# Kernel optimization log

Measured on AMD Instinct MI355X. Metric: run time of the kernel, lower is better.

Reference implementation:

```python
import jax, jax.numpy as jnp
import numpy as np

SEQ, B, IN, H = 256, 64, 1024, 1024
P_IN, P_HID = 0.3, 0.3


def setup_inputs() -> dict:
    key = jax.random.key(0)
    ks = jax.random.split(key, 8)
    bound = 1.0 / np.sqrt(H)
    # variational dropout masks: Bernoulli(keep)/keep, sampled once, reused every step
    keep_x, keep_h = 1.0 - P_IN, 1.0 - P_HID
    mask_x = (jax.random.uniform(ks[0], (B, IN)) < keep_x).astype(jnp.float32) / keep_x
    mask_h = (jax.random.uniform(ks[1], (B, H)) < keep_h).astype(jnp.float32) / keep_h
    return {
        "x": jax.random.normal(ks[2], (SEQ, B, IN), jnp.float32),
        "h0": jax.random.normal(ks[3], (B, H), jnp.float32),
        "c0": jax.random.normal(ks[4], (B, H), jnp.float32),
        "mask_x": mask_x,
        "mask_h": mask_h,
        "W_ih": jax.random.uniform(ks[5], (4 * H, IN), jnp.float32, -bound, bound),
        "W_hh": jax.random.uniform(ks[6], (4 * H, H), jnp.float32, -bound, bound),
        "b_ih": jax.random.uniform(ks[7], (4 * H,), jnp.float32, -bound, bound),
        "b_hh": jax.random.uniform(jax.random.fold_in(key, 9), (4 * H,), jnp.float32, -bound, bound),
    }


def reference(x, h0, c0, mask_x, mask_h, W_ih, W_hh, b_ih, b_hh):
    # input dropout mask applied once to all timesteps, then input gate
    # projections precomputed in one big GEMM: [S, B, 4H]
    x_gates = jnp.einsum('sbi,gi->sbg', x * mask_x[None], W_ih) + (b_ih + b_hh)

    def step(carry, xg):
        h, c = carry
        # hidden dropout mask applied to h before the cell, every step
        gates = xg + (h * mask_h) @ W_hh.T  # [B, 4H]
        i, f, g, o = jnp.split(gates, 4, axis=-1)  # torch LSTM gate order
        i = jax.nn.sigmoid(i)
        f = jax.nn.sigmoid(f)
        g = jnp.tanh(g)
        o = jax.nn.sigmoid(o)
        c_new = f * c + i * g
        h_new = o * jnp.tanh(c_new)
        return (h_new, c_new), h_new

    (h_n, c_n), output = jax.lax.scan(step, (h0, c0), x_gates)
    return output, h_n, c_n
```

## Files before the change

kernel.cpp:

```cpp
#include <hip/hip_runtime.h>
#include <stdint.h>
#include <stddef.h>


#define SEQ 256

typedef __attribute__((ext_vector_type(8))) __bf16 bf16x8;
typedef __attribute__((ext_vector_type(4))) float  f32x4;
typedef __attribute__((ext_vector_type(4))) _Float16 f16x4;
typedef __attribute__((ext_vector_type(4))) unsigned int u32x4;
typedef unsigned short u16;
typedef unsigned int   u32;
typedef unsigned long long u64;

__device__ __forceinline__ u16 f2bf(float f) {
  union { float f; unsigned u; } v; v.f = f;
  unsigned r = v.u + 0x7FFFu + ((v.u >> 16) & 1u);
  return (u16)(r >> 16);
}
__device__ __forceinline__ float sigm(float x) {
  return __builtin_amdgcn_rcpf(1.f + __expf(-x));
}
__device__ __forceinline__ float tanh_fast(float x) {
  float xc = fminf(15.f, fmaxf(-15.f, x));
  float t = __expf(-2.f * xc);
  return (1.f - t) * __builtin_amdgcn_rcpf(1.f + t);
}
__device__ __forceinline__ float pick4(int idx, float v0, float v1, float v2, float v3) {
  float lo = (idx & 1) ? v1 : v0;
  float hi = (idx & 1) ? v3 : v2;
  return (idx & 2) ? hi : lo;
}


__global__ __launch_bounds__(256) void prep_kernel(
    const float* __restrict__ x, const float* __restrict__ h0,
    const float* __restrict__ c0, const float* __restrict__ mask_x,
    const float* __restrict__ mask_h, const float* __restrict__ Wih,
    const float* __restrict__ Whh, const float* __restrict__ bih,
    const float* __restrict__ bhh,
    u16* __restrict__ Wihp, u16* __restrict__ Whhp, u16* __restrict__ Ap,
    u16* __restrict__ mhp0, float* __restrict__ bias, float* __restrict__ c,
    u32* __restrict__ flags, int persist)
{
  const unsigned t    = blockIdx.x * 256u + threadIdx.x;
  const unsigned idx8 = t * 8u;

  union Pack8 { u16 o[8]; u32x4 v; };

  {
    const unsigned l   = (idx8 >> 3) & 63u;
    const unsigned kwg = (idx8 >> 9) & 31u;
    const unsigned m   = (idx8 >> 14) & 3u;
    const unsigned s   = idx8 >> 16;
    const unsigned b   = m * 16u + (l & 15u);
    const unsigned k   = kwg * 32u + (l >> 4) * 8u;
    const float* xp = &x[((size_t)s * 64u + b) * 1024u + k];
    const float* mp = &mask_x[b * 1024u + k];
    Pack8 p;
    #pragma unroll
    for (int e = 0; e < 8; ++e) p.o[e] = f2bf(xp[e] * mp[e]);
    *(u32x4*)&Ap[idx8] = p.v;
  }
  if (t < 524288u) {
    const unsigned l   = (idx8 >> 3) & 63u;
    const unsigned kcw = (idx8 >> 9) & 31u;
    const unsigned wb  = idx8 >> 14;
    const unsigned nl  = l & 15u;
    const unsigned n   = (nl & 3u) * 1024u + wb * 4u + (nl >> 2);
    const unsigned k   = kcw * 32u + (l >> 4) * 8u;
    const float* wip = &Wih[n * 1024u + k];
    const float* whp = &Whh[n * 1024u + k];
    Pack8 pi, ph;
    #pragma unroll
    for (int e = 0; e < 8; ++e) { pi.o[e] = f2bf(wip[e]); ph.o[e] = f2bf(whp[e]); }
    *(u32x4*)&Wihp[idx8] = pi.v;
    *(u32x4*)&Whhp[idx8] = ph.v;
  }
  if (t < 8192u) {
    const unsigned l   = (idx8 >> 3) & 63u;
    const unsigned kwg = (idx8 >> 9) & 31u;
    const unsigned m   = idx8 >> 14;
    const unsigned b   = m * 16u + (l & 15u);
    const unsigned k   = kwg * 32u + (l >> 4) * 8u;
    const float* hp = &h0[b * 1024u + k];
    const float* mp = &mask_h[b * 1024u + k];
    Pack8 p;
    #pragma unroll
    for (int e = 0; e < 8; ++e) p.o[e] = f2bf(hp[e] * mp[e]);
    *(u32x4*)&mhp0[idx8] = p.v;
    *(f32x4*)&c[idx8]     = *(const f32x4*)&c0[idx8];
    *(f32x4*)&c[idx8 + 4] = *(const f32x4*)&c0[idx8 + 4];
  }
  if (t < 512u) {
    #pragma unroll
    for (int e = 0; e < 8; ++e) bias[idx8 + e] = bih[idx8 + e] + bhh[idx8 + e];
  }
  if (persist && t < 256u) flags[t] = 0u;
}

__global__ __launch_bounds__(512) void lstm_persist(
    const u16* __restrict__ Ap, const u16* __restrict__ Wihp,
    const u16* __restrict__ Whhp, const float* __restrict__ bias,
    const float* __restrict__ c0, const float* __restrict__ mask_h,
    u16* __restrict__ mh_seq,
    u32* __restrict__ flags, float* __restrict__ out)
{
  __shared__ f32x4 lds[8][4][64];
  __shared__ u32 cnt;

  const int tid = threadIdx.x;
  const int w   = tid >> 6;
  const int l   = tid & 63;
  const int bk  = blockIdx.x;
  const int rg  = bk >> 6;
  const int cg  = bk & 63;

  const bf16x8* WHV = (const bf16x8*)Whhp;
  const bf16x8* WIV = (const bf16x8*)Wihp;
  const bf16x8* ApV = (const bf16x8*)Ap;

  bf16x8 wh[4][4], wi[4][4];
  #pragma unroll
  for (int nt = 0; nt < 4; ++nt)
    #pragma unroll
    for (int kw = 0; kw < 4; ++kw) {
      wh[nt][kw] = WHV[((cg * 4 + nt) * 32 + w * 4 + kw) * 64 + l];
      wi[nt][kw] = WIV[((cg * 4 + nt) * 32 + w * 4 + kw) * 64 + l];
    }

  const int nl     = l & 15;
  const int quad   = l >> 4;
  const int g_role = nl & 3;
  const int jh     = nl >> 2;

  const int nt_e  = w & 3;
  const int rb    = (w >> 2) * 2;
  const int col_h = cg * 16 + nt_e * 4 + jh;
  const float bias_reg = bias[g_role * 1024 + col_h];
  float c_reg[2], mask_reg[2];
  #pragma unroll
  for (int rl = 0; rl < 2; ++rl) {
    const int row = rg * 16 + quad * 4 + rb + rl;
    c_reg[rl]    = c0[row * 1024 + col_h];
    mask_reg[rl] = mask_h[row * 1024 + col_h];
  }

  const int mh_u16_base =
      ((rg * 32 + (cg >> 1)) * 64 + ((cg & 1) * 2 + (nt_e >> 1)) * 16 + quad * 4) * 8
      + (nt_e & 1) * 4;

  const u32 poll_off = (u32)((rg * 64 + w * 8 + (l & 7)) * 4);

  if (tid == 0) cnt = 0u;
  __syncthreads();

  for (int s = 0; s < SEQ; ++s) {
    const u16* mi = mh_seq + (size_t)s * 65536;
    u16*       mo = mh_seq + (size_t)(s + 1) * 65536;

    f32x4 acc[4];
    #pragma unroll
    for (int nt = 0; nt < 4; ++nt) acc[nt] = (f32x4){0.f, 0.f, 0.f, 0.f};
    #pragma unroll
    for (int kw = 0; kw < 4; ++kw) {
      bf16x8 a = ApV[((s * 4 + rg) * 32 + w * 4 + kw) * 64 + l];
      #pragma unroll
      for (int nt = 0; nt < 4; ++nt)
        acc[nt] = __builtin_amdgcn_mfma_f32_16x16x32_bf16(a, wi[nt][kw], acc[nt], 0, 0, 0);
    }

    if (s > 0) {
      const u32 target = (u32)s;
      int spins = 0;
      for (;;) {
        u32 f;
        asm volatile("global_load_dword %0, %1, %2 sc0 sc1\n\t"
                     "s_waitcnt vmcnt(0)"
                     : "=v"(f) : "v"(poll_off), "s"(flags) : "memory");
        if (__all(f >= target)) break;
        if (++spins > (1 << 15)) break;
        __builtin_amdgcn_s_sleep(1);
      }
    }

    union { u32x4 r; bf16x8 v; } hf[4];
    #pragma unroll
    for (int kw = 0; kw < 4; ++kw) {
      const u32 off = (u32)(((rg * 32 + w * 4 + kw) * 64 + l) * 16);
      asm volatile("global_load_dwordx4 %0, %1, %2 sc0 sc1"
                   : "=v"(hf[kw].r) : "v"(off), "s"(mi) : "memory");
    }
    asm volatile("s_waitcnt vmcnt(0)" ::: "memory");
    __builtin_amdgcn_sched_barrier(0);
    #pragma unroll
    for (int kw = 0; kw < 4; ++kw)
      #pragma unroll
      for (int nt = 0; nt < 4; ++nt)
        acc[nt] = __builtin_amdgcn_mfma_f32_16x16x32_bf16(hf[kw].v, wh[nt][kw], acc[nt], 0, 0, 0);

    #pragma unroll
    for (int nt = 0; nt < 4; ++nt) lds[w][nt][l] = acc[nt];
    __syncthreads();

    f32x4 t = lds[0][nt_e][l];
    #pragma unroll
    for (int ww = 1; ww < 8; ++ww) t += lds[ww][nt_e][l];

    f32x4 ho_s[2];
    f32x4 co_s[2];
    #pragma unroll
    for (int rl = 0; rl < 2; ++rl) {
      const int r = rb + rl;
      const float gp = t[r] + bias_reg;
      const float v1 = __shfl_xor(gp, 1, 64);
      const float v2 = __shfl_xor(gp, 2, 64);
      const float v3 = __shfl_xor(gp, 3, 64);
      const float ig = pick4(g_role,     gp, v1, v2, v3);
      const float fg = pick4(g_role ^ 1, gp, v1, v2, v3);
      const float gg = pick4(g_role ^ 2, gp, v1, v2, v3);
      const float og = pick4(g_role ^ 3, gp, v1, v2, v3);
      const float iv = sigm(ig);
      const float fv = sigm(fg);
      const float gv = tanh_fast(gg);
      const float ov = sigm(og);
      const float cn = fv * c_reg[rl] + iv * gv;
      c_reg[rl] = cn;
      const float hn = ov * tanh_fast(cn);
      const float mv = hn * mask_reg[rl];

      const float h1 = __shfl_xor(hn, 4, 64);
      const float h2 = __shfl_xor(hn, 8, 64);
      const float h3 = __shfl_xor(hn, 12, 64);
      const float m1 = __shfl_xor(mv, 4, 64);
      const float m2 = __shfl_xor(mv, 8, 64);
      const float m3 = __shfl_xor(mv, 12, 64);
      ho_s[rl] = (f32x4){hn, h1, h2, h3};
      if (s == SEQ - 1) {
        const float cn1 = __shfl_xor(cn, 4, 64);
        const float cn2 = __shfl_xor(cn, 8, 64);
        const float cn3 = __shfl_xor(cn, 12, 64);
        co_s[rl] = (f32x4){cn, cn1, cn2, cn3};
      }
      if (nl == 0) {
        const u64 pk = (u64)f2bf(mv) | ((u64)f2bf(m1) << 16)
                     | ((u64)f2bf(m2) << 32) | ((u64)f2bf(m3) << 48);
        __hip_atomic_store((u64*)&mo[mh_u16_base + r * 8], pk,
                           __ATOMIC_RELAXED, __HIP_MEMORY_SCOPE_AGENT);
      }
    }
    asm volatile("s_waitcnt vmcnt(0)" ::: "memory");
    u32 old = 0u;
    if (l == 0)
      old = __hip_atomic_fetch_add(&cnt, 1u, __ATOMIC_RELAXED, __HIP_MEMORY_SCOPE_WORKGROUP);
    if (l == 0 && old == 7u) {
      __hip_atomic_store(&cnt, 0u, __ATOMIC_RELAXED, __HIP_MEMORY_SCOPE_WORKGROUP);
      if (s < SEQ - 1) {
        u32 val  = (u32)(s + 1);
        u32 voff = (u32)(bk * 4);
        asm volatile("global_store_dword %0, %1, %2 sc0 sc1"
                     :: "v"(voff), "v"(val), "s"(flags) : "memory");
      }
    }
    if (nl == 0) {
      #pragma unroll
      for (int rl = 0; rl < 2; ++rl) {
        const int row = rg * 16 + quad * 4 + rb + rl;
        *(f32x4*)&out[((size_t)s * 64 + row) * 1024 + cg * 16 + nt_e * 4] = ho_s[rl];
        if (s == SEQ - 1) {
          *(f32x4*)&out[16777216 + row * 1024 + cg * 16 + nt_e * 4] = ho_s[rl];
          *(f32x4*)&out[16777216 + 65536 + row * 1024 + cg * 16 + nt_e * 4] = co_s[rl];
        }
      }
    }
    __syncthreads();
  }
}

__global__ __launch_bounds__(256) void lstm_step(
    const u16* __restrict__ Ap,
    const u16* __restrict__ Wihp,
    const u16* __restrict__ Whhp,
    const _Float16* __restrict__ xg,
    const float* __restrict__ bias,
    const u16* __restrict__ mh_in, u16* __restrict__ mh_out,
    float* __restrict__ c, const float* __restrict__ mask_h,
    float* __restrict__ out, int s)
{
  __shared__ f32x4 lds[4][4][64];

  const int tid = threadIdx.x;
  const int w   = tid >> 6;
  const int l   = tid & 63;
  const int bk  = blockIdx.x;

  const bf16x8* mb = (const bf16x8*)mh_in;
  const bf16x8* WH = (const bf16x8*)Whhp;

  f32x4 acc[4] = { {0,0,0,0}, {0,0,0,0}, {0,0,0,0}, {0,0,0,0} };

  #pragma unroll 2
  for (int kw = 0; kw < 8; ++kw) {
    bf16x8 b = WH[(bk * 32 + w * 8 + kw) * 64 + l];
    #pragma unroll
    for (int m = 0; m < 4; ++m) {
      bf16x8 a = mb[(m * 32 + w * 8 + kw) * 64 + l];
      acc[m] = __builtin_amdgcn_mfma_f32_16x16x32_bf16(a, b, acc[m], 0, 0, 0);
    }
  }
  if (xg == nullptr) {
    const bf16x8* ApV = (const bf16x8*)Ap;
    const bf16x8* WI  = (const bf16x8*)Wihp;
    #pragma unroll 2
    for (int kw = 0; kw < 8; ++kw) {
      bf16x8 b = WI[(bk * 32 + w * 8 + kw) * 64 + l];
      #pragma unroll
      for (int m = 0; m < 4; ++m) {
        bf16x8 a = ApV[((s * 4 + m) * 32 + w * 8 + kw) * 64 + l];
        acc[m] = __builtin_amdgcn_mfma_f32_16x16x32_bf16(a, b, acc[m], 0, 0, 0);
      }
    }
  }
  #pragma unroll
  for (int m = 0; m < 4; ++m) lds[w][m][l] = acc[m];
  __syncthreads();

  f32x4 t = lds[0][w][l];
  #pragma unroll
  for (int ww = 1; ww < 4; ++ww) t += lds[ww][w][l];

  const int nl     = l & 15;
  const int quad   = l >> 4;
  const int g_role = nl & 3;
  const int jh     = nl >> 2;
  const int col_h  = bk * 4 + jh;

  if (xg != nullptr) {
    f16x4 xv = *(const f16x4*)&xg[((((size_t)s * 256 + bk) * 4 + w) * 64 + l) * 4];
    #pragma unroll
    for (int r = 0; r < 4; ++r) t[r] += (float)xv[r];
  }
  const float bias_reg = bias[g_role * 1024 + col_h];
  const int kwg = col_h >> 5;
  const int lp  = ((col_h >> 3) & 3) * 16;

  #pragma unroll
  for (int r = 0; r < 4; ++r) {
    const int b_row = w * 16 + quad * 4 + r;
    const float gp = t[r] + bias_reg;
    const float v1 = __shfl_xor(gp, 1, 64);
    const float v2 = __shfl_xor(gp, 2, 64);
    const float v3 = __shfl_xor(gp, 3, 64);
    const float ig = pick4(g_role,     gp, v1, v2, v3);
    const float fg = pick4(g_role ^ 1, gp, v1, v2, v3);
    const float gg = pick4(g_role ^ 2, gp, v1, v2, v3);
    const float og = pick4(g_role ^ 3, gp, v1, v2, v3);
    const float iv = sigm(ig);
    const float fv = sigm(fg);
    const float gv = tanh_fast(gg);
    const float ov = sigm(og);
    const float cold = c[b_row * 1024 + col_h];
    const float cn = fv * cold + iv * gv;
    const float hn = ov * tanh_fast(cn);
    if (g_role == 0) {
      c[b_row * 1024 + col_h] = cn;
      out[((size_t)s * 64 + b_row) * 1024 + col_h] = hn;
      mh_out[((w * 32 + kwg) * 64 + (lp + (b_row & 15))) * 8 + (col_h & 7)] =
          f2bf(hn * mask_h[b_row * 1024 + col_h]);
      if (s == SEQ - 1) {
        out[16777216 + b_row * 1024 + col_h] = hn;
        out[16777216 + 65536 + b_row * 1024 + col_h] = cn;
      }
    }
  }
}

extern "C" void kernel_launch(void* const* d_in, const int* in_sizes, int n_in,
                              void* d_out, int out_size, void* d_ws, size_t ws_size,
                              hipStream_t stream)
{
  const float* x      = (const float*)d_in[0];
  const float* h0     = (const float*)d_in[1];
  const float* c0     = (const float*)d_in[2];
  const float* mask_x = (const float*)d_in[3];
  const float* mask_h = (const float*)d_in[4];
  const float* Wih    = (const float*)d_in[5];
  const float* Whh    = (const float*)d_in[6];
  const float* bih    = (const float*)d_in[7];
  const float* bhh    = (const float*)d_in[8];
  float* out = (float*)d_out;

  char* ws = (char*)d_ws;
  u16*   Wihp   = (u16*)(ws + 0);
  u16*   Whhp   = (u16*)(ws + 8388608);
  u16*   Ap     = (u16*)(ws + 16777216);
  u16*   mh0    = (u16*)(ws + 50331648);
  u16*   mh1    = (u16*)(ws + 50462720);
  float* bias   = (float*)(ws + 50593792);
  float* c      = (float*)(ws + 50610176);
  u32*   flags  = (u32*)(ws + 50872320);
  u16*   mh_seq = (u16*)(ws + 50873344);
  const bool persist = (ws_size >= (size_t)84558848);

  u16* mh_init = persist ? mh_seq : mh0;

  hipLaunchKernelGGL(prep_kernel, dim3(8192), dim3(256), 0, stream,
                     x, h0, c0, mask_x, mask_h, Wih, Whh, bih, bhh,
                     Wihp, Whhp, Ap, mh_init, bias, c, flags, (int)persist);

  if (persist) {
    hipLaunchKernelGGL(lstm_persist, dim3(256), dim3(512), 0, stream,
                       Ap, Wihp, Whhp, bias, c0, mask_h, mh_seq, flags, out);
  } else {
    for (int s = 0; s < SEQ; ++s) {
      const u16* mi = (s & 1) ? mh1 : mh0;
      u16*       mo = (s & 1) ? mh0 : mh1;
      hipLaunchKernelGGL(lstm_step, dim3(256), dim3(256), 0, stream,
                         Ap, Wihp, Whhp, (const _Float16*)nullptr, bias, mi, mo,
                         c, mask_h, out, s);
    }
  }
}
```

Before: 956.4 us.

## Replace flag-based inter-block barrier with sentinel-poisoned data polling

Removes the per-block step flags and the workgroup counter. The prep kernel now fills the hidden-state sequence buffer with 0xFFFF sentinels, and each wave polls the actual hidden-state data it needs, reissuing loads only for chunks that still show the sentinel. LDS accumulation is double-buffered so the trailing __syncthreads can be dropped. This is meant to take the flag store/poll round trip and a barrier off the critical path of each recurrent step. The risks are extra prep writes across the whole sequence buffer, and correctness that depends on the bf16 sentinel never appearing as a real value and on the 8-byte stores being seen atomically.

Result: slower. 1.850 ms (+93.4%).

```diff
diff --git a/kernel.cpp b/kernel.cpp
--- a/kernel.cpp
+++ b/kernel.cpp
@@ -41,7 +41,7 @@
     const float* __restrict__ bhh,
     u16* __restrict__ Wihp, u16* __restrict__ Whhp, u16* __restrict__ Ap,
     u16* __restrict__ mhp0, float* __restrict__ bias, float* __restrict__ c,
-    u32* __restrict__ flags, int persist)
+    u16* __restrict__ mh_seq, int persist)
 {
   const unsigned t    = blockIdx.x * 256u + threadIdx.x;
   const unsigned idx8 = t * 8u;
@@ -62,6 +62,10 @@
     for (int e = 0; e < 8; ++e) p.o[e] = f2bf(xp[e] * mp[e]);
     *(u32x4*)&Ap[idx8] = p.v;
   }
+  if (persist) {
+    u32x4 ones = {0xFFFFFFFFu, 0xFFFFFFFFu, 0xFFFFFFFFu, 0xFFFFFFFFu};
+    *(u32x4*)&mh_seq[65536u + idx8] = ones;
+  }
   if (t < 524288u) {
     const unsigned l   = (idx8 >> 3) & 63u;
     const unsigned kcw = (idx8 >> 9) & 31u;
@@ -96,18 +100,15 @@
     #pragma unroll
     for (int e = 0; e < 8; ++e) bias[idx8 + e] = bih[idx8 + e] + bhh[idx8 + e];
   }
-  if (persist && t < 256u) flags[t] = 0u;
 }
 
 __global__ __launch_bounds__(512) void lstm_persist(
     const u16* __restrict__ Ap, const u16* __restrict__ Wihp,
     const u16* __restrict__ Whhp, const float* __restrict__ bias,
     const float* __restrict__ c0, const float* __restrict__ mask_h,
-    u16* __restrict__ mh_seq,
-    u32* __restrict__ flags, float* __restrict__ out)
+    u16* __restrict__ mh_seq, float* __restrict__ out)
 {
-  __shared__ f32x4 lds[8][4][64];
-  __shared__ u32 cnt;
+  __shared__ f32x4 lds[2][8][4][64];
 
   const int tid = threadIdx.x;
   const int w   = tid >> 6;
@@ -150,14 +151,20 @@
       ((rg * 32 + (cg >> 1)) * 64 + ((cg & 1) * 2 + (nt_e >> 1)) * 16 + quad * 4) * 8
       + (nt_e & 1) * 4;
 
-  const u32 poll_off = (u32)((rg * 64 + w * 8 + (l & 7)) * 4);
-
-  if (tid == 0) cnt = 0u;
   __syncthreads();
 
   for (int s = 0; s < SEQ; ++s) {
     const u16* mi = mh_seq + (size_t)s * 65536;
     u16*       mo = mh_seq + (size_t)(s + 1) * 65536;
+    const int  p  = s & 1;
+
+    union { u32x4 r; bf16x8 v; } hf[4];
+    #pragma unroll
+    for (int kw = 0; kw < 4; ++kw) {
+      const u32 off = (u32)(((rg * 32 + w * 4 + kw) * 64 + l) * 16);
+      asm volatile("global_load_dwordx4 %0, %1, %2 sc0 sc1"
+                   : "=v"(hf[kw].r) : "v"(off), "s"(mi) : "memory");
+    }
 
     f32x4 acc[4];
     #pragma unroll
@@ -170,29 +177,31 @@
         acc[nt] = __builtin_amdgcn_mfma_f32_16x16x32_bf16(a, wi[nt][kw], acc[nt], 0, 0, 0);
     }
 
-    if (s > 0) {
-      const u32 target = (u32)s;
+    {
       int spins = 0;
       for (;;) {
-        u32 f;
-        asm volatile("global_load_dword %0, %1, %2 sc0 sc1\n\t"
-                     "s_waitcnt vmcnt(0)"
-                     : "=v"(f) : "v"(poll_off), "s"(flags) : "memory");
-        if (__all(f >= target)) break;
-        if (++spins > (1 << 15)) break;
-        __builtin_amdgcn_s_sleep(1);
-      }
-    }
-
-    union { u32x4 r; bf16x8 v; } hf[4];
-    #pragma unroll
-    for (int kw = 0; kw < 4; ++kw) {
-      const u32 off = (u32)(((rg * 32 + w * 4 + kw) * 64 + l) * 16);
-      asm volatile("global_load_dwordx4 %0, %1, %2 sc0 sc1"
-                   : "=v"(hf[kw].r) : "v"(off), "s"(mi) : "memory");
-    }
-    asm volatile("s_waitcnt vmcnt(0)" ::: "memory");
-    __builtin_amdgcn_sched_barrier(0);
+        asm volatile("s_waitcnt vmcnt(0)" ::: "memory");
+        __builtin_amdgcn_sched_barrier(0);
+        int b0 = ((hf[0].r[0] & 0xFFFFu) == 0xFFFFu) | ((hf[0].r[2] & 0xFFFFu) == 0xFFFFu);
+        int b1 = ((hf[1].r[0] & 0xFFFFu) == 0xFFFFu) | ((hf[1].r[2] & 0xFFFFu) == 0xFFFFu);
+        int b2 = ((hf[2].r[0] & 0xFFFFu) == 0xFFFFu) | ((hf[2].r[2] & 0xFFFFu) == 0xFFFFu);
+        int b3 = ((hf[3].r[0] & 0xFFFFu) == 0xFFFFu) | ((hf[3].r[2] & 0xFFFFu) == 0xFFFFu);
+        if (!__any(b0 | b1 | b2 | b3)) break;
+        if (++spins > (1 << 14)) break;
+        if (spins > 8) __builtin_amdgcn_s_sleep(1);
+        const int rebad[4] = { b0, b1, b2, b3 };
+        #pragma unroll
+        for (int kw = 0; kw < 4; ++kw) {
+          if (__any(rebad[kw])) {
+            const u32 off = (u32)(((rg * 32 + w * 4 + kw) * 64 + l) * 16);
+            asm volatile("global_load_dwordx4 %0, %1, %2 sc0 sc1"
+                         : "=v"(hf[kw].r) : "v"(off), "s"(mi) : "memory");
+          }
+        }
+      }
+      __builtin_amdgcn_sched_barrier(0);
+    }
+
     #pragma unroll
     for (int kw = 0; kw < 4; ++kw)
       #pragma unroll
@@ -200,12 +209,12 @@
         acc[nt] = __builtin_amdgcn_mfma_f32_16x16x32_bf16(hf[kw].v, wh[nt][kw], acc[nt], 0, 0, 0);
 
     #pragma unroll
-    for (int nt = 0; nt < 4; ++nt) lds[w][nt][l] = acc[nt];
+    for (int nt = 0; nt < 4; ++nt) lds[p][w][nt][l] = acc[nt];
     __syncthreads();
 
-    f32x4 t = lds[0][nt_e][l];
-    #pragma unroll
-    for (int ww = 1; ww < 8; ++ww) t += lds[ww][nt_e][l];
+    f32x4 t = lds[p][0][nt_e][l];
+    #pragma unroll
+    for (int ww = 1; ww < 8; ++ww) t += lds[p][ww][nt_e][l];
 
     f32x4 ho_s[2];
     f32x4 co_s[2];
@@ -249,19 +258,6 @@
                            __ATOMIC_RELAXED, __HIP_MEMORY_SCOPE_AGENT);
       }
     }
-    asm volatile("s_waitcnt vmcnt(0)" ::: "memory");
-    u32 old = 0u;
-    if (l == 0)
-      old = __hip_atomic_fetch_add(&cnt, 1u, __ATOMIC_RELAXED, __HIP_MEMORY_SCOPE_WORKGROUP);
-    if (l == 0 && old == 7u) {
-      __hip_atomic_store(&cnt, 0u, __ATOMIC_RELAXED, __HIP_MEMORY_SCOPE_WORKGROUP);
-      if (s < SEQ - 1) {
-        u32 val  = (u32)(s + 1);
-        u32 voff = (u32)(bk * 4);
-        asm volatile("global_store_dword %0, %1, %2 sc0 sc1"
-                     :: "v"(voff), "v"(val), "s"(flags) : "memory");
-      }
-    }
     if (nl == 0) {
       #pragma unroll
       for (int rl = 0; rl < 2; ++rl) {
@@ -273,7 +269,6 @@
         }
       }
     }
-    __syncthreads();
   }
 }
 
@@ -398,7 +393,6 @@
   u16*   mh1    = (u16*)(ws + 50462720);
   float* bias   = (float*)(ws + 50593792);
   float* c      = (float*)(ws + 50610176);
-  u32*   flags  = (u32*)(ws + 50872320);
   u16*   mh_seq = (u16*)(ws + 50873344);
   const bool persist = (ws_size >= (size_t)84558848);
 
@@ -406,11 +400,11 @@
 
   hipLaunchKernelGGL(prep_kernel, dim3(8192), dim3(256), 0, stream,
                      x, h0, c0, mask_x, mask_h, Wih, Whh, bih, bhh,
-                     Wihp, Whhp, Ap, mh_init, bias, c, flags, (int)persist);
+                     Wihp, Whhp, Ap, mh_init, bias, c, mh_seq, (int)persist);
 
   if (persist) {
     hipLaunchKernelGGL(lstm_persist, dim3(256), dim3(512), 0, stream,
-                       Ap, Wihp, Whhp, bias, c0, mask_h, mh_seq, flags, out);
+                       Ap, Wihp, Whhp, bias, c0, mask_h, mh_seq, out);
   } else {
     for (int s = 0; s < SEQ; ++s) {
       const u16* mi = (s & 1) ? mh1 : mh0;
```
